# Performance work log

Hardware: AMD Instinct MI355X
Metric: run time of the kernel (lower is better)

The kernel has to match this reference:

```python
import jax, jax.numpy as jnp
import numpy as np

K = 3  # kernel size
PAD = K // 2


def setup_inputs() -> dict:
    key = jax.random.key(0)
    k1, k2, k3 = jax.random.split(key, 3)
    B, C, H, W = 8, 192, 128, 128
    x = jax.random.normal(k1, (B, C, H, W), dtype=jnp.float32)
    kernel = 0.02 * jax.random.normal(k2, (C, K * K), dtype=jnp.float32)
    gate_w = 0.02 * jax.random.normal(k3, (C,), dtype=jnp.float32)
    gate_b = jnp.zeros((C,), dtype=jnp.float32)
    return {"x": x, "kernel": kernel, "gate_w": gate_w, "gate_b": gate_b}


def reference(x, kernel, gate_w, gate_b):
    B, C, H, W = x.shape
    # F.unfold with zero padding: patches[b,c,ki*K+kj,h,w] = x_pad[b,c,h+ki,w+kj]
    xp = jnp.pad(x, ((0, 0), (0, 0), (PAD, PAD), (PAD, PAD)))
    patches = jnp.stack(
        [xp[:, :, i:i + H, j:j + W] for i in range(K) for j in range(K)],
        axis=2,
    )  # [B, C, K*K, H, W]
    # depthwise 1x1 gate: per-channel scale + bias, then sigmoid
    theta = jax.nn.sigmoid(x * gate_w[None, :, None, None] + gate_b[None, :, None, None])
    # max-plus: max_v [ f(u-v) + theta(u) * k(v) ]
    scored = patches + theta[:, :, None] * kernel[None, :, :, None, None]
    return jnp.max(scored, axis=2)  # [B, C, H, W]
```

## Files before the change

kernel.cpp:

```cpp
#include <hip/hip_runtime.h>
#include <math.h>

#define BB 8
#define CC 192
#define HH 128
#define WW 128
#define RPT 16

struct RowReg { float l; float4 v; float r; };

__device__ __forceinline__ RowReg load_row(const float* __restrict__ xp,
                                           int g, int col, int wg) {
    float4 v;
    if (g >= 0 && g < HH) {
        v = *(const float4*)(xp + g * WW + col);
    } else {
        v = make_float4(0.0f, 0.0f, 0.0f, 0.0f);
    }
    float l = __shfl_up(v.w, 1);
    float r = __shfl_down(v.x, 1);
    RowReg rr;
    rr.l = (wg == 0)  ? 0.0f : l;
    rr.r = (wg == 31) ? 0.0f : r;
    rr.v = v;
    return rr;
}

__device__ __forceinline__ float col9(float a0, float a1, float a2,
                                      float b0, float b1, float b2,
                                      float c0, float c1, float c2,
                                      float th, const float* kk) {
    float m;
    m = fmaf(th, kk[0], a0);
    m = fmaxf(m, fmaf(th, kk[1], a1));
    m = fmaxf(m, fmaf(th, kk[2], a2));
    m = fmaxf(m, fmaf(th, kk[3], b0));
    m = fmaxf(m, fmaf(th, kk[4], b1));
    m = fmaxf(m, fmaf(th, kk[5], b2));
    m = fmaxf(m, fmaf(th, kk[6], c0));
    m = fmaxf(m, fmaf(th, kk[7], c1));
    m = fmaxf(m, fmaf(th, kk[8], c2));
    return m;
}

__global__ __launch_bounds__(256) void dynmorph_kernel(
    const float* __restrict__ x,
    const float* __restrict__ kern,
    const float* __restrict__ gw,
    const float* __restrict__ gb,
    float* __restrict__ out)
{
    const int tid  = threadIdx.x;
    const int lane = tid & 63;
    const int wg   = lane & 31;
    const int rs   = (tid >> 6) * 2 + (lane >> 5);
    const int col  = wg * 4;
    const int r0   = rs * RPT;

    const int bc = blockIdx.x;
    const int c  = bc % CC;

    const float* xp = x   + (size_t)bc * (HH * WW);
    float*       op = out + (size_t)bc * (HH * WW);

    float kk[9];
#pragma unroll
    for (int i = 0; i < 9; ++i) kk[i] = kern[c * 9 + i];
    const float gwc = gw[c];
    const float gbc = gb[c];

    RowReg A = load_row(xp, r0 - 1, col, wg);
    RowReg B = load_row(xp, r0,     col, wg);

#pragma unroll 4
    for (int g = 0; g < RPT; ++g) {
        const int gr = r0 + g;
        RowReg C = load_row(xp, gr + 1, col, wg);

        float t0 = 1.0f / (1.0f + __expf(-fmaf(B.v.x, gwc, gbc)));
        float t1 = 1.0f / (1.0f + __expf(-fmaf(B.v.y, gwc, gbc)));
        float t2 = 1.0f / (1.0f + __expf(-fmaf(B.v.z, gwc, gbc)));
        float t3 = 1.0f / (1.0f + __expf(-fmaf(B.v.w, gwc, gbc)));

        float4 o;
        o.x = col9(A.l,   A.v.x, A.v.y,
                   B.l,   B.v.x, B.v.y,
                   C.l,   C.v.x, C.v.y, t0, kk);
        o.y = col9(A.v.x, A.v.y, A.v.z,
                   B.v.x, B.v.y, B.v.z,
                   C.v.x, C.v.y, C.v.z, t1, kk);
        o.z = col9(A.v.y, A.v.z, A.v.w,
                   B.v.y, B.v.z, B.v.w,
                   C.v.y, C.v.z, C.v.w, t2, kk);
        o.w = col9(A.v.z, A.v.w, A.r,
                   B.v.z, B.v.w, B.r,
                   C.v.z, C.v.w, C.r,   t3, kk);

        *(float4*)(op + gr * WW + col) = o;

        A = B;
        B = C;
    }
}

extern "C" void kernel_launch(void* const* d_in, const int* in_sizes, int n_in,
                              void* d_out, int out_size, void* d_ws, size_t ws_size,
                              hipStream_t stream) {
    const float* x    = (const float*)d_in[0];
    const float* kern = (const float*)d_in[1];
    const float* gw   = (const float*)d_in[2];
    const float* gb   = (const float*)d_in[3];
    float* out        = (float*)d_out;

    dim3 grid(BB * CC);
    dim3 block(256);
    dynmorph_kernel<<<grid, block, 0, stream>>>(x, kern, gw, gb, out);
}
```

Before: 185.9 us.

## Preload all strip rows up front and split each plane across two blocks

Each thread now issues all of its row loads (RPT+2 float4s) before any compute, then does the halo shuffles and the unrolled compute loop. Previously each load was serialized with that row's compute. Rows per thread drop from 16 to 8, and the grid gains a second dimension so two blocks cover each 128-row plane. This should expose more memory-level parallelism and double the block count. It costs more registers per thread and a higher halo reload ratio, up to 10 rows loaded per 8 rows output.

```diff
diff --git a/kernel.cpp b/kernel.cpp
--- a/kernel.cpp
+++ b/kernel.cpp
@@ -5,26 +5,7 @@
 #define CC 192
 #define HH 128
 #define WW 128
-#define RPT 16
-
-struct RowReg { float l; float4 v; float r; };
-
-__device__ __forceinline__ RowReg load_row(const float* __restrict__ xp,
-                                           int g, int col, int wg) {
-    float4 v;
-    if (g >= 0 && g < HH) {
-        v = *(const float4*)(xp + g * WW + col);
-    } else {
-        v = make_float4(0.0f, 0.0f, 0.0f, 0.0f);
-    }
-    float l = __shfl_up(v.w, 1);
-    float r = __shfl_down(v.x, 1);
-    RowReg rr;
-    rr.l = (wg == 0)  ? 0.0f : l;
-    rr.r = (wg == 31) ? 0.0f : r;
-    rr.v = v;
-    return rr;
-}
+#define RPT 8
 
 __device__ __forceinline__ float col9(float a0, float a1, float a2,
                                       float b0, float b1, float b2,
@@ -55,7 +36,7 @@
     const int wg   = lane & 31;
     const int rs   = (tid >> 6) * 2 + (lane >> 5);
     const int col  = wg * 4;
-    const int r0   = rs * RPT;
+    const int r0   = blockIdx.y * (RPT * 8) + rs * RPT;
 
     const int bc = blockIdx.x;
     const int c  = bc % CC;
@@ -69,37 +50,50 @@
     const float gwc = gw[c];
     const float gbc = gb[c];
 
-    RowReg A = load_row(xp, r0 - 1, col, wg);
-    RowReg B = load_row(xp, r0,     col, wg);
+    float4 v[RPT + 2];
+#pragma unroll
+    for (int i = 0; i < RPT + 2; ++i) {
+        const int g = r0 - 1 + i;
+        if (g >= 0 && g < HH) {
+            v[i] = *(const float4*)(xp + g * WW + col);
+        } else {
+            v[i] = make_float4(0.0f, 0.0f, 0.0f, 0.0f);
+        }
+    }
 
-#pragma unroll 4
+    float lf[RPT + 2], rt[RPT + 2];
+#pragma unroll
+    for (int i = 0; i < RPT + 2; ++i) {
+        const float l = __shfl_up(v[i].w, 1);
+        const float r = __shfl_down(v[i].x, 1);
+        lf[i] = (wg == 0)  ? 0.0f : l;
+        rt[i] = (wg == 31) ? 0.0f : r;
+    }
+
+#pragma unroll
     for (int g = 0; g < RPT; ++g) {
-        const int gr = r0 + g;
-        RowReg C = load_row(xp, gr + 1, col, wg);
+        const float4 A = v[g], B = v[g + 1], Cv = v[g + 2];
 
-        float t0 = 1.0f / (1.0f + __expf(-fmaf(B.v.x, gwc, gbc)));
-        float t1 = 1.0f / (1.0f + __expf(-fmaf(B.v.y, gwc, gbc)));
-        float t2 = 1.0f / (1.0f + __expf(-fmaf(B.v.z, gwc, gbc)));
-        float t3 = 1.0f / (1.0f + __expf(-fmaf(B.v.w, gwc, gbc)));
+        const float t0 = 1.0f / (1.0f + __expf(-fmaf(B.x, gwc, gbc)));
+        const float t1 = 1.0f / (1.0f + __expf(-fmaf(B.y, gwc, gbc)));
+        const float t2 = 1.0f / (1.0f + __expf(-fmaf(B.z, gwc, gbc)));
+        const float t3 = 1.0f / (1.0f + __expf(-fmaf(B.w, gwc, gbc)));
 
         float4 o;
-        o.x = col9(A.l,   A.v.x, A.v.y,
-                   B.l,   B.v.x, B.v.y,
-                   C.l,   C.v.x, C.v.y, t0, kk);
-        o.y = col9(A.v.x, A.v.y, A.v.z,
-                   B.v.x, B.v.y, B.v.z,
-                   C.v.x, C.v.y, C.v.z, t1, kk);
-        o.z = col9(A.v.y, A.v.z, A.v.w,
-                   B.v.y, B.v.z, B.v.w,
-                   C.v.y, C.v.z, C.v.w, t2, kk);
-        o.w = col9(A.v.z, A.v.w, A.r,
-                   B.v.z, B.v.w, B.r,
-                   C.v.z, C.v.w, C.r,   t3, kk);
+        o.x = col9(lf[g],  A.x, A.y,
+                   lf[g+1], B.x, B.y,
+                   lf[g+2], Cv.x, Cv.y, t0, kk);
+        o.y = col9(A.x, A.y, A.z,
+                   B.x, B.y, B.z,
+                   Cv.x, Cv.y, Cv.z, t1, kk);
+        o.z = col9(A.y, A.z, A.w,
+                   B.y, B.z, B.w,
+                   Cv.y, Cv.z, Cv.w, t2, kk);
+        o.w = col9(A.z, A.w, rt[g],
+                   B.z, B.w, rt[g+1],
+                   Cv.z, Cv.w, rt[g+2], t3, kk);
 
-        *(float4*)(op + gr * WW + col) = o;
-
-        A = B;
-        B = C;
+        *(float4*)(op + (r0 + g) * WW + col) = o;
     }
 }
 
@@ -112,7 +106,7 @@
     const float* gb   = (const float*)d_in[3];
     float* out        = (float*)d_out;
 
-    dim3 grid(BB * CC);
+    dim3 grid(BB * CC, 2);
     dim3 block(256);
     dynmorph_kernel<<<grid, block, 0, stream>>>(x, kern, gw, gb, out);
 }
```

After: 185.6 us. Within noise of the previous version (-0.2%).
